# Performance work log

Measured on AMD Instinct MI355X. Metric: run time of the kernel, lower is better.

## Reference

```python
import jax, jax.numpy as jnp
import numpy as np

CHANNELS = [(3, 64), (64, 64), (64, 128), (128, 128), (128, 256), (256, 256), (256, 256),
            (256, 512), (512, 512), (512, 512), (512, 512), (512, 512), (512, 512)]
HW = 256
IN_FEAT = 512 * (HW // 32) * (HW // 32)  # 32768


def _conv(x, w):
    # 3x3, stride 1, pad 1, NCHW / OIHW, no bias
    return jax.lax.conv_general_dilated(x, w, (1, 1), ((1, 1), (1, 1)),
                                         dimension_numbers=("NCHW", "OIHW", "NCHW"))


def _maxpool2(x):
    return jax.lax.reduce_window(x, -jnp.inf, jax.lax.max, (1, 1, 2, 2), (1, 1, 2, 2), "VALID")


def setup_inputs() -> dict:
    key = jax.random.key(0)
    keys = jax.random.split(key, 17)
    inp = {"x": jax.random.normal(keys[0], (1, 3, HW, HW), jnp.float32),
           "H": HW, "W": HW, "nTh": 32, "nTw": 32}
    for i, (cin, cout) in enumerate(CHANNELS):
        scale = (1.0 / np.sqrt(9.0 * cin)).astype(np.float32) if hasattr(np.sqrt(9.0 * cin), 'astype') else 1.0 / np.sqrt(9.0 * cin)
        inp[f"cw{i + 1}"] = jax.random.normal(keys[1 + i], (cout, cin, 3, 3), jnp.float32) * np.float32(1.0 / np.sqrt(9.0 * cin))
    inp["fw1"] = jax.random.normal(keys[14], (4096, IN_FEAT), jnp.float32) * np.float32(1.0 / np.sqrt(IN_FEAT))
    inp["fw2"] = jax.random.normal(keys[15], (4096, 4096), jnp.float32) * np.float32(1.0 / np.sqrt(4096))
    inp["fw3"] = jax.random.normal(keys[16], (1000, 4096), jnp.float32) * np.float32(1.0 / np.sqrt(4096))
    return inp


def reference(x, H, W, nTh, nTw, cw1, cw2, cw3, cw4, cw5, cw6, cw7, cw8, cw9, cw10,
              cw11, cw12, cw13, fw1, fw2, fw3):
    # VGG-16 conv stack; tiling in the original is an execution schedule only,
    # the math equals the untiled stack. conv -> relu repeated, maxpool per block.
    conv_ws = [cw1, cw2, cw3, cw4, cw5, cw6, cw7, cw8, cw9, cw10, cw11, cw12, cw13]
    blocks = [(0, 2), (2, 4), (4, 7), (7, 10), (10, 13)]
    h = x
    for lo, hi in blocks:
        for w in conv_ws[lo:hi]:
            h = jax.nn.relu(_conv(h, w))
        h = _maxpool2(h)
    h = h.reshape(h.shape[0], -1)          # [1, 32768]
    h = h @ fw1.T                           # fc1 (no bias, no relu, as in source)
    h = h @ fw2.T                           # fc2
    h = h @ fw3.T                           # fc3 -> [1, 1000]
    return h
```

## Files before the change

kernel.cpp:

```cpp
#include <hip/hip_runtime.h>
#include <cstddef>


typedef __attribute__((ext_vector_type(8))) short short8;
typedef __attribute__((ext_vector_type(4))) float f32x4;

__device__ inline unsigned short f2bf(float f) {
    unsigned int u = __builtin_bit_cast(unsigned int, f);
    u += 0x7FFF + ((u >> 16) & 1);
    return (unsigned short)(u >> 16);
}
__device__ inline float bf2f(unsigned short h) {
    unsigned int u = ((unsigned int)h) << 16;
    return __builtin_bit_cast(float, u);
}

__global__ void wt_transform_k(const float* __restrict__ w, unsigned short* __restrict__ wt,
                               int Cin, int Cout)
{
    const int co = blockIdx.x, pos = blockIdx.y;
    for (int ci = threadIdx.x; ci < Cin; ci += 64)
        wt[(size_t)(pos * Cout + co) * Cin + ci] = f2bf(w[(size_t)(co * Cin + ci) * 9 + pos]);
}

template<int PR, int MODE>
__global__ __launch_bounds__(256, 2)
void conv_mfma_k(const unsigned short* __restrict__ act,
                 const unsigned short* __restrict__ wt,
                 void* __restrict__ outp,
                 int Cin, int Cout, int H, int W, int chunkCi)
{
    constexpr int NT = PR / 4;
    constexpr int ICELLS = (PR + 2) * 18;
    __shared__ __align__(16) unsigned short wLds[9 * 64 * 32];
    __shared__ __align__(16) unsigned short iLds[ICELLS * 32];

    const int tid = threadIdx.x;
    const int lane = tid & 63, wv = tid >> 6;
    const int half = lane >> 4, l15 = lane & 15;
    const int tilesX = W >> 4;
    const int pY = blockIdx.x / tilesX, pX = blockIdx.x - pY * tilesX;
    const int y0 = pY * PR, x0 = pX * 16;
    const int cob = blockIdx.y, s = blockIdx.z;
    const int ciBeg = s * chunkCi, ciEnd = ciBeg + chunkCi;

    f32x4 acc[4][NT];
#pragma unroll
    for (int mt = 0; mt < 4; ++mt)
#pragma unroll
        for (int nt = 0; nt < NT; ++nt) acc[mt][nt] = (f32x4){0.f, 0.f, 0.f, 0.f};

    for (int ci0 = ciBeg; ci0 < ciEnd; ci0 += 32) {
        __syncthreads();
#pragma unroll
        for (int it = 0; it < 9; ++it) {
            const int idx = it * 256 + tid;
            const int cell = idx >> 2, q = idx & 3;
            const int pos = cell >> 6, co = cell & 63;
            const uint4 v = *(const uint4*)(wt +
                (size_t)(pos * Cout + (cob << 6) + co) * Cin + ci0 + q * 8);
            *(uint4*)&wLds[cell * 32 + q * 8] = v;
        }
#pragma unroll
        for (int it = 0; it < (ICELLS * 4 + 255) / 256; ++it) {
            const int idx = it * 256 + tid;
            if (idx < ICELLS * 4) {
                const int cell = idx >> 2, q = idx & 3;
                const int r = cell / 18, c = cell - r * 18;
                const int y = y0 - 1 + r, x = x0 - 1 + c;
                uint4 v = {0u, 0u, 0u, 0u};
                if (y >= 0 && y < H && x >= 0 && x < W)
                    v = *(const uint4*)(act + (size_t)(y * W + x) * Cin + ci0 + q * 8);
                *(uint4*)&iLds[cell * 32 + q * 8] = v;
            }
        }
        __syncthreads();
#pragma unroll
        for (int ky = 0; ky < 3; ++ky)
#pragma unroll
        for (int kx = 0; kx < 3; ++kx) {
            const int pos = ky * 3 + kx;
            short8 a[4];
#pragma unroll
            for (int mt = 0; mt < 4; ++mt)
                a[mt] = *(const short8*)&wLds[((pos << 6) + (mt << 4) + l15) * 32 + half * 8];
#pragma unroll
            for (int nt = 0; nt < NT; ++nt) {
                const short8 b = *(const short8*)
                    &iLds[((wv * NT + nt + ky) * 18 + l15 + kx) * 32 + half * 8];
#pragma unroll
                for (int mt = 0; mt < 4; ++mt)
                    acc[mt][nt] = __builtin_amdgcn_mfma_f32_16x16x32_bf16(a[mt], b, acc[mt][nt], 0, 0, 0);
            }
        }
    }

    const int xg = x0 + l15;
#pragma unroll
    for (int mt = 0; mt < 4; ++mt)
#pragma unroll
    for (int nt = 0; nt < NT; ++nt) {
        const int yg = y0 + wv * NT + nt;
        const int co = (cob << 6) + (mt << 4) + half * 4;
        const size_t base = (size_t)(yg * W + xg) * Cout + co;
        if (MODE == 2) {
            float4 v = make_float4(acc[mt][nt][0], acc[mt][nt][1], acc[mt][nt][2], acc[mt][nt][3]);
            *(float4*)((float*)outp + (size_t)s * Cout * H * W + base) = v;
        } else {
            ushort4 u;
            u.x = f2bf(MODE == 0 ? fmaxf(acc[mt][nt][0], 0.f) : acc[mt][nt][0]);
            u.y = f2bf(MODE == 0 ? fmaxf(acc[mt][nt][1], 0.f) : acc[mt][nt][1]);
            u.z = f2bf(MODE == 0 ? fmaxf(acc[mt][nt][2], 0.f) : acc[mt][nt][2]);
            u.w = f2bf(MODE == 0 ? fmaxf(acc[mt][nt][3], 0.f) : acc[mt][nt][3]);
            *(ushort4*)((unsigned short*)outp + base) = u;
        }
    }
}

#define TILE 16
#define COB  32
__global__ __launch_bounds__(256)
void conv1_k(const float* __restrict__ in, const float* __restrict__ wt,
             unsigned short* __restrict__ out)
{
    const int Cin = 3, H = 256, W = 256, HW = H * W;
    __shared__ float sIn[2][648];
    __shared__ float sWt[2][768];

    const int tid = threadIdx.x;
    const int bx = blockIdx.x, by = blockIdx.y, co_blk = blockIdx.z;
    const int co_grp = tid >> 6;
    const int lane = tid & 63;
    const int tx = lane & 7, ty = lane >> 3;
    const int x0 = bx * TILE, y0 = by * TILE;

    int iLdsI[3], iG[3], iSub[3]; bool iOk[3];
    int wLdsI[3], wG[3], wSub[3]; bool wOk[3];
#pragma unroll
    for (int j = 0; j < 3; ++j) {
        int i = tid + j * 256;
        iOk[j] = false; iLdsI[j] = 0; iG[j] = 0; iSub[j] = 0;
        if (i < 648) {
            int sub = i / 324; int r = i - sub * 324;
            int iy = r / 18;   int ix = r - iy * 18;
            iSub[j] = sub; iLdsI[j] = sub * 324 + r;
            int y = y0 - 1 + iy, x = x0 - 1 + ix;
            if (y >= 0 && y < H && x >= 0 && x < W) { iOk[j] = true; iG[j] = sub * HW + y * W + x; }
        }
        wOk[j] = false; wLdsI[j] = 0; wG[j] = 0; wSub[j] = 0;
        if (i < 576) {
            int sub = i / 288; int r = i - sub * 288;
            int col = r / 9;   int k = r - col * 9;
            wSub[j] = sub; wLdsI[j] = sub * 384 + col * 12 + k;
            wG[j] = ((co_blk * COB + col) * Cin + sub) * 9 + k;
            wOk[j] = true;
        }
    }

    float4 acc[8];
#pragma unroll
    for (int c = 0; c < 8; ++c) acc[c] = make_float4(0.f, 0.f, 0.f, 0.f);

    const int nSteps = 2;
    float rIn[3], rWt[3];
    {
#pragma unroll
        for (int j = 0; j < 3; ++j)
            rIn[j] = (iOk[j] && iSub[j] < 3) ? in[iG[j]] : 0.f;
#pragma unroll
        for (int j = 0; j < 3; ++j)
            rWt[j] = (wOk[j] && wSub[j] < 3) ? wt[wG[j]] : 0.f;
#pragma unroll
        for (int j = 0; j < 3; ++j) { if (tid + j * 256 < 648) sIn[0][iLdsI[j]] = rIn[j]; }
#pragma unroll
        for (int j = 0; j < 3; ++j) { if (tid + j * 256 < 576) sWt[0][wLdsI[j]] = rWt[j]; }
    }

    for (int t = 0; t < nSteps; ++t) {
        __syncthreads();
        const bool more = (t + 1) < nSteps;
        if (more) {
            const int ci0 = 2;
#pragma unroll
            for (int j = 0; j < 3; ++j)
                rIn[j] = (iOk[j] && (ci0 + iSub[j]) < 3) ? in[(size_t)ci0 * HW + iG[j]] : 0.f;
#pragma unroll
            for (int j = 0; j < 3; ++j)
                rWt[j] = (wOk[j] && (ci0 + wSub[j]) < 3) ? wt[(size_t)ci0 * 9 + wG[j]] : 0.f;
        }
        const int buf = t & 1;
        const float* sI = sIn[buf];
        const float* sW = sWt[buf];
#pragma unroll
        for (int sub = 0; sub < 2; ++sub) {
            float wv[4][4];
            const float* sp = sI + sub * 324 + (2 * ty) * 18 + 2 * tx;
#pragma unroll
            for (int r = 0; r < 4; ++r) {
                float2 a = *(const float2*)(sp + r * 18);
                float2 b = *(const float2*)(sp + r * 18 + 2);
                wv[r][0] = a.x; wv[r][1] = a.y; wv[r][2] = b.x; wv[r][3] = b.y;
            }
#pragma unroll
            for (int c = 0; c < 8; ++c) {
                const float* wp = sW + sub * 384 + (co_grp * 8 + c) * 12;
                float4 w0 = *(const float4*)wp;
                float4 w1 = *(const float4*)(wp + 4);
                float  w8 = wp[8];
                const float wk[9] = {w0.x, w0.y, w0.z, w0.w, w1.x, w1.y, w1.z, w1.w, w8};
                float* ac = (float*)&acc[c];
#pragma unroll
                for (int py = 0; py < 2; ++py)
#pragma unroll
                for (int px = 0; px < 2; ++px) {
                    float sacc = ac[py * 2 + px];
#pragma unroll
                    for (int kk = 0; kk < 9; ++kk)
                        sacc = fmaf(wv[py + kk / 3][px + kk % 3], wk[kk], sacc);
                    ac[py * 2 + px] = sacc;
                }
            }
        }
        if (more) {
#pragma unroll
            for (int j = 0; j < 3; ++j) { if (tid + j * 256 < 648) sIn[buf ^ 1][iLdsI[j]] = rIn[j]; }
#pragma unroll
            for (int j = 0; j < 3; ++j) { if (tid + j * 256 < 576) sWt[buf ^ 1][wLdsI[j]] = rWt[j]; }
        }
    }

    const int co0 = co_blk * COB + co_grp * 8;
#pragma unroll
    for (int py = 0; py < 2; ++py)
#pragma unroll
    for (int px = 0; px < 2; ++px) {
        const int y = y0 + 2 * ty + py, x = x0 + 2 * tx + px;
        unsigned short u8[8];
#pragma unroll
        for (int c = 0; c < 8; ++c)
            u8[c] = f2bf(fmaxf(((const float*)&acc[c])[py * 2 + px], 0.f));
        *(uint4*)(out + (size_t)(y * W + x) * 64 + co0) = *(uint4*)u8;
    }
}

__global__ __launch_bounds__(256)
void pool_cvt_k(const unsigned short* __restrict__ P, unsigned short* __restrict__ out,
                int C, int H, int W)
{
    const int C8 = C >> 3, Wo = W >> 1, Ho = H >> 1;
    const int n = Ho * Wo * C8;
    int i = blockIdx.x * 256 + threadIdx.x;
    if (i >= n) return;
    const int c8 = i % C8, p = i / C8;
    const int yo = p / Wo, xo = p - yo * Wo;
    const size_t b = (size_t)(2 * yo * W + 2 * xo) * C + c8 * 8;
    uint4 a0 = *(const uint4*)(P + b);
    uint4 a1 = *(const uint4*)(P + b + C);
    uint4 a2 = *(const uint4*)(P + b + (size_t)W * C);
    uint4 a3 = *(const uint4*)(P + b + (size_t)W * C + C);
    const unsigned short* s0 = (const unsigned short*)&a0;
    const unsigned short* s1 = (const unsigned short*)&a1;
    const unsigned short* s2 = (const unsigned short*)&a2;
    const unsigned short* s3 = (const unsigned short*)&a3;
    unsigned short u8[8];
#pragma unroll
    for (int k = 0; k < 8; ++k) {
        float m = fmaxf(fmaxf(bf2f(s0[k]), bf2f(s1[k])), fmaxf(bf2f(s2[k]), bf2f(s3[k])));
        u8[k] = f2bf(fmaxf(m, 0.f));
    }
    *(uint4*)(out + (size_t)p * C + c8 * 8) = *(uint4*)u8;
}

__global__ __launch_bounds__(256)
void reduce_cvt_k(const float* __restrict__ P, unsigned short* __restrict__ out,
                  int n4, int S)
{
    int i = blockIdx.x * 256 + threadIdx.x;
    if (i >= n4) return;
    const float4* p4 = (const float4*)P;
    float4 a = p4[i];
    for (int s = 1; s < S; ++s) {
        float4 b = p4[(size_t)i + (size_t)s * n4];
        a.x += b.x; a.y += b.y; a.z += b.z; a.w += b.w;
    }
    ushort4 u;
    u.x = f2bf(fmaxf(a.x, 0.f)); u.y = f2bf(fmaxf(a.y, 0.f));
    u.z = f2bf(fmaxf(a.z, 0.f)); u.w = f2bf(fmaxf(a.w, 0.f));
    *(ushort4*)(out + (size_t)i * 4) = u;
}

__global__ __launch_bounds__(256)
void reduce_pool_cvt_k(const float* __restrict__ P, unsigned short* __restrict__ out,
                       int C, int H, int W, int S)
{
    const int C4 = C >> 2, Wo = W >> 1, Ho = H >> 1;
    const int n = Ho * Wo * C4;
    int i = blockIdx.x * 256 + threadIdx.x;
    if (i >= n) return;
    const int c4 = i % C4, p = i / C4;
    const int yo = p / Wo, xo = p - yo * Wo;
    const size_t CHW = (size_t)C * H * W;
    const size_t b = (size_t)(2 * yo * W + 2 * xo) * C + c4 * 4;
    float4 v[4] = {{0,0,0,0},{0,0,0,0},{0,0,0,0},{0,0,0,0}};
    for (int s = 0; s < S; ++s) {
        const float* ps = P + s * CHW;
        float4 t0 = *(const float4*)(ps + b);
        float4 t1 = *(const float4*)(ps + b + C);
        float4 t2 = *(const float4*)(ps + b + (size_t)W * C);
        float4 t3 = *(const float4*)(ps + b + (size_t)W * C + C);
        v[0].x += t0.x; v[0].y += t0.y; v[0].z += t0.z; v[0].w += t0.w;
        v[1].x += t1.x; v[1].y += t1.y; v[1].z += t1.z; v[1].w += t1.w;
        v[2].x += t2.x; v[2].y += t2.y; v[2].z += t2.z; v[2].w += t2.w;
        v[3].x += t3.x; v[3].y += t3.y; v[3].z += t3.z; v[3].w += t3.w;
    }
    ushort4 u;
    u.x = f2bf(fmaxf(fmaxf(fmaxf(v[0].x, v[1].x), fmaxf(v[2].x, v[3].x)), 0.f));
    u.y = f2bf(fmaxf(fmaxf(fmaxf(v[0].y, v[1].y), fmaxf(v[2].y, v[3].y)), 0.f));
    u.z = f2bf(fmaxf(fmaxf(fmaxf(v[0].z, v[1].z), fmaxf(v[2].z, v[3].z)), 0.f));
    u.w = f2bf(fmaxf(fmaxf(fmaxf(v[0].w, v[1].w), fmaxf(v[2].w, v[3].w)), 0.f));
    *(ushort4*)(out + (size_t)p * C + c4 * 4) = u;
}

__global__ __launch_bounds__(256)
void reduce_pool_f32_k(const float* __restrict__ P, float* __restrict__ out,
                       int C, int H, int W, int S)
{
    const int Wo = W >> 1, Ho = H >> 1;
    const int n = Ho * Wo * C;
    int i = blockIdx.x * 256 + threadIdx.x;
    if (i >= n) return;
    const int c = i % C, p = i / C;
    const int yo = p / Wo, xo = p - yo * Wo;
    const size_t CHW = (size_t)C * H * W;
    float v0 = 0.f, v1 = 0.f, v2 = 0.f, v3 = 0.f;
    const size_t b = (size_t)(2 * yo * W + 2 * xo) * C + c;
    for (int s = 0; s < S; ++s) {
        const float* ps = P + s * CHW;
        v0 += ps[b]; v1 += ps[b + C]; v2 += ps[b + (size_t)W * C]; v3 += ps[b + (size_t)W * C + C];
    }
    out[(size_t)c * (Ho * Wo) + p] = fmaxf(fmaxf(fmaxf(v0, v1), fmaxf(v2, v3)), 0.f);
}

__global__ __launch_bounds__(256)
void gemv_k(const float* __restrict__ Wm, const float* __restrict__ xv,
            float* __restrict__ y, int K)
{
    __shared__ float red[4];
    const int tid = threadIdx.x;
    const float4* row = (const float4*)(Wm + (size_t)blockIdx.x * K);
    const float4* x4  = (const float4*)xv;
    const int K4 = K >> 2;
    float sum = 0.f;
    for (int i = tid; i < K4; i += 256) {
        float4 a = row[i], b = x4[i];
        sum += a.x * b.x + a.y * b.y + a.z * b.z + a.w * b.w;
    }
#pragma unroll
    for (int off = 32; off > 0; off >>= 1) sum += __shfl_down(sum, off, 64);
    if ((tid & 63) == 0) red[tid >> 6] = sum;
    __syncthreads();
    if (tid == 0) y[blockIdx.x] = red[0] + red[1] + red[2] + red[3];
}

extern "C" void kernel_launch(void* const* d_in, const int* in_sizes, int n_in,
                              void* d_out, int out_size, void* d_ws, size_t ws_size,
                              hipStream_t stream)
{
    (void)in_sizes; (void)n_in; (void)out_size; (void)ws_size;
    const float* x = (const float*)d_in[0];
    const float* cw[13];
    for (int i = 0; i < 13; ++i) cw[i] = (const float*)d_in[5 + i];
    const float* fw1 = (const float*)d_in[18];
    const float* fw2 = (const float*)d_in[19];
    const float* fw3 = (const float*)d_in[20];
    float* outp = (float*)d_out;

    static const int CIN[12]  = {64, 64, 128, 128, 256, 256, 256, 512, 512, 512, 512, 512};
    static const int COUT[12] = {64, 128, 128, 256, 256, 256, 512, 512, 512, 512, 512, 512};

    char* ws = (char*)d_ws;
    size_t wOff[12]; size_t o = 0;
    for (int i = 0; i < 12; ++i) { wOff[i] = o; o += (size_t)9 * COUT[i] * CIN[i]; }
    unsigned short* WT = (unsigned short*)ws;
    size_t ao = (o * 2 + 255) & ~(size_t)255;
    unsigned short* bA = (unsigned short*)(ws + ao);
    unsigned short* bB = (unsigned short*)(ws + ao + 8388608);
    char* Pr = ws + ao + 2 * 8388608;
    unsigned short* Pu = (unsigned short*)Pr;
    float* Pf = (float*)Pr;
    float* fcIn = (float*)bA;
    float* F1 = (float*)bB;
    float* F2 = F1 + 4096;

    for (int i = 0; i < 12; ++i)
        wt_transform_k<<<dim3(COUT[i], 9), 64, 0, stream>>>(cw[i + 1], WT + wOff[i], CIN[i], COUT[i]);

    conv1_k<<<dim3(16, 16, 2), 256, 0, stream>>>(x, cw[0], bA);

    conv_mfma_k<16, 1><<<dim3(256, 1, 1), 256, 0, stream>>>(bA, WT + wOff[0], Pu, 64, 64, 256, 256, 64);
    pool_cvt_k<<<(128 * 128 * 8 + 255) / 256, 256, 0, stream>>>(Pu, bB, 64, 256, 256);
    conv_mfma_k<8, 0><<<dim3(128, 2, 1), 256, 0, stream>>>(bB, WT + wOff[1], bA, 64, 128, 128, 128, 64);
    conv_mfma_k<8, 1><<<dim3(128, 2, 1), 256, 0, stream>>>(bA, WT + wOff[2], Pu, 128, 128, 128, 128, 128);
    pool_cvt_k<<<(64 * 64 * 16 + 255) / 256, 256, 0, stream>>>(Pu, bB, 128, 128, 128);
    conv_mfma_k<8, 2><<<dim3(32, 4, 2), 256, 0, stream>>>(bB, WT + wOff[3], Pf, 128, 256, 64, 64, 64);
    reduce_cvt_k<<<(262144 + 255) / 256, 256, 0, stream>>>(Pf, bA, 262144, 2);
    conv_mfma_k<8, 2><<<dim3(32, 4, 2), 256, 0, stream>>>(bA, WT + wOff[4], Pf, 256, 256, 64, 64, 128);
    reduce_cvt_k<<<(262144 + 255) / 256, 256, 0, stream>>>(Pf, bB, 262144, 2);
    conv_mfma_k<8, 2><<<dim3(32, 4, 2), 256, 0, stream>>>(bB, WT + wOff[5], Pf, 256, 256, 64, 64, 128);
    reduce_pool_cvt_k<<<(65536 + 255) / 256, 256, 0, stream>>>(Pf, bA, 256, 64, 64, 2);
    conv_mfma_k<8, 2><<<dim3(8, 8, 4), 256, 0, stream>>>(bA, WT + wOff[6], Pf, 256, 512, 32, 32, 64);
    reduce_cvt_k<<<(131072 + 255) / 256, 256, 0, stream>>>(Pf, bB, 131072, 4);
    conv_mfma_k<8, 2><<<dim3(8, 8, 4), 256, 0, stream>>>(bB, WT + wOff[7], Pf, 512, 512, 32, 32, 128);
    reduce_cvt_k<<<(131072 + 255) / 256, 256, 0, stream>>>(Pf, bA, 131072, 4);
    conv_mfma_k<8, 2><<<dim3(8, 8, 4), 256, 0, stream>>>(bA, WT + wOff[8], Pf, 512, 512, 32, 32, 128);
    reduce_pool_cvt_k<<<(32768 + 255) / 256, 256, 0, stream>>>(Pf, bB, 512, 32, 32, 4);
    conv_mfma_k<8, 2><<<dim3(2, 8, 16), 256, 0, stream>>>(bB, WT + wOff[9], Pf, 512, 512, 16, 16, 32);
    reduce_cvt_k<<<(32768 + 255) / 256, 256, 0, stream>>>(Pf, bA, 32768, 16);
    conv_mfma_k<8, 2><<<dim3(2, 8, 16), 256, 0, stream>>>(bA, WT + wOff[10], Pf, 512, 512, 16, 16, 32);
    reduce_cvt_k<<<(32768 + 255) / 256, 256, 0, stream>>>(Pf, bB, 32768, 16);
    conv_mfma_k<8, 2><<<dim3(2, 8, 16), 256, 0, stream>>>(bB, WT + wOff[11], Pf, 512, 512, 16, 16, 32);
    reduce_pool_f32_k<<<(32768 + 255) / 256, 256, 0, stream>>>(Pf, fcIn, 512, 16, 16, 16);

    gemv_k<<<4096, 256, 0, stream>>>(fw1, fcIn, F1, 32768);
    gemv_k<<<4096, 256, 0, stream>>>(fw2, F1, F2, 4096);
    gemv_k<<<1000, 256, 0, stream>>>(fw3, F2, outp, 4096);
}
```

Baseline: 1.037 ms.

## Double-buffer conv LDS via direct global-to-LDS loads, fuse pooling, batch weight transform

```diff
diff --git a/kernel.cpp b/kernel.cpp
--- a/kernel.cpp
+++ b/kernel.cpp
@@ -15,25 +15,69 @@
     return __builtin_bit_cast(float, u);
 }
 
-__global__ void wt_transform_k(const float* __restrict__ w, unsigned short* __restrict__ wt,
-                               int Cin, int Cout)
-{
-    const int co = blockIdx.x, pos = blockIdx.y;
-    for (int ci = threadIdx.x; ci < Cin; ci += 64)
-        wt[(size_t)(pos * Cout + co) * Cin + ci] = f2bf(w[(size_t)(co * Cin + ci) * 9 + pos]);
+__device__ __forceinline__ void gl_lds16(const void* src, unsigned m0v) {
+    asm volatile("s_mov_b32 m0, %1\n\t"
+                 "global_load_lds_dwordx4 %0, off"
+                 :: "v"(src), "s"(m0v) : "memory");
+}
+
+struct WtDesc { const float* src; unsigned dst; int cin; int cout; int blk0; };
+struct WtArgs { WtDesc d[12]; };
+
+__global__ __launch_bounds__(256)
+void wt_all_k(WtArgs A, unsigned short* __restrict__ wt, unsigned short* __restrict__ guard)
+{
+    __shared__ unsigned short lds[4][9 * 520];
+    const int tid = threadIdx.x, wv = tid >> 6, lane = tid & 63;
+    if (blockIdx.x == 0 && tid < 128) guard[tid] = 0;
+
+    int l = 0;
+#pragma unroll
+    for (int i = 1; i < 12; ++i) l = ((int)blockIdx.x >= A.d[i].blk0) ? i : l;
+    const WtDesc D = A.d[l];
+    const int co = ((int)blockIdx.x - D.blk0) * 4 + wv;
+    const int n = D.cin * 9;
+    const int cinP = D.cin + 8;
+
+    const float4* src = (const float4*)(D.src + (size_t)co * n);
+    for (int i = lane; i < (n >> 2); i += 64) {
+        float4 v = src[i];
+        unsigned short b[4] = {f2bf(v.x), f2bf(v.y), f2bf(v.z), f2bf(v.w)};
+        const int f0 = i * 4;
+#pragma unroll
+        for (int k = 0; k < 4; ++k) {
+            const int f = f0 + k, ci = f / 9, pos = f - ci * 9;
+            lds[wv][pos * cinP + ci] = b[k];
+        }
+    }
+    __syncthreads();
+    unsigned short* dstb = wt + D.dst;
+#pragma unroll 1
+    for (int pos = 0; pos < 9; ++pos) {
+        unsigned short* drow = dstb + ((size_t)pos * D.cout + co) * D.cin;
+        for (int c4 = lane; c4 < (D.cin >> 2); c4 += 64) {
+            ushort4 u = *(const ushort4*)&lds[wv][pos * cinP + c4 * 4];
+            *(ushort4*)(drow + c4 * 4) = u;
+        }
+    }
 }
 
 template<int PR, int MODE>
-__global__ __launch_bounds__(256, 2)
+__global__ __launch_bounds__(256)
 void conv_mfma_k(const unsigned short* __restrict__ act,
                  const unsigned short* __restrict__ wt,
+                 const unsigned short* __restrict__ guard,
                  void* __restrict__ outp,
                  int Cin, int Cout, int H, int W, int chunkCi)
 {
     constexpr int NT = PR / 4;
     constexpr int ICELLS = (PR + 2) * 18;
-    __shared__ __align__(16) unsigned short wLds[9 * 64 * 32];
-    __shared__ __align__(16) unsigned short iLds[ICELLS * 32];
+    constexpr int ITIN = (ICELLS * 4 + 255) / 256;
+    constexpr int VL = 9 + ITIN;
+    static_assert(VL == 12 || VL == 15, "unexpected stage depth");
+
+    __shared__ __align__(16) unsigned short wLds[2][9 * 64 * 32];
+    __shared__ __align__(16) unsigned short iLds[2][ITIN * 2048];
 
     const int tid = threadIdx.x;
     const int lane = tid & 63, wv = tid >> 6;
@@ -42,7 +86,8 @@
     const int pY = blockIdx.x / tilesX, pX = blockIdx.x - pY * tilesX;
     const int y0 = pY * PR, x0 = pX * 16;
     const int cob = blockIdx.y, s = blockIdx.z;
-    const int ciBeg = s * chunkCi, ciEnd = ciBeg + chunkCi;
+    const int ciBeg = s * chunkCi;
+    const int nCh = chunkCi >> 5;
 
     f32x4 acc[4][NT];
 #pragma unroll
@@ -50,31 +95,46 @@
 #pragma unroll
         for (int nt = 0; nt < NT; ++nt) acc[mt][nt] = (f32x4){0.f, 0.f, 0.f, 0.f};
 
-    for (int ci0 = ciBeg; ci0 < ciEnd; ci0 += 32) {
-        __syncthreads();
+    auto STAGE = [&](int buf, int ci0) {
+        const unsigned wB = (unsigned)(size_t)&wLds[buf][0];
+        const unsigned iB = (unsigned)(size_t)&iLds[buf][0];
 #pragma unroll
         for (int it = 0; it < 9; ++it) {
             const int idx = it * 256 + tid;
             const int cell = idx >> 2, q = idx & 3;
             const int pos = cell >> 6, co = cell & 63;
-            const uint4 v = *(const uint4*)(wt +
-                (size_t)(pos * Cout + (cob << 6) + co) * Cin + ci0 + q * 8);
-            *(uint4*)&wLds[cell * 32 + q * 8] = v;
-        }
-#pragma unroll
-        for (int it = 0; it < (ICELLS * 4 + 255) / 256; ++it) {
+            const unsigned short* src = wt +
+                (size_t)(pos * Cout + (cob << 6) + co) * Cin + ci0 + q * 8;
+            gl_lds16(src, __builtin_amdgcn_readfirstlane(wB + (unsigned)(it * 4096 + wv * 1024)));
+        }
+#pragma unroll
+        for (int it = 0; it < ITIN; ++it) {
             const int idx = it * 256 + tid;
-            if (idx < ICELLS * 4) {
-                const int cell = idx >> 2, q = idx & 3;
-                const int r = cell / 18, c = cell - r * 18;
-                const int y = y0 - 1 + r, x = x0 - 1 + c;
-                uint4 v = {0u, 0u, 0u, 0u};
-                if (y >= 0 && y < H && x >= 0 && x < W)
-                    v = *(const uint4*)(act + (size_t)(y * W + x) * Cin + ci0 + q * 8);
-                *(uint4*)&iLds[cell * 32 + q * 8] = v;
-            }
-        }
-        __syncthreads();
+            const int cell = idx >> 2, q = idx & 3;
+            const int r = cell / 18, c = cell - r * 18;
+            const int y = y0 - 1 + r, x = x0 - 1 + c;
+            const bool ok = (idx < ICELLS * 4) & (y >= 0) & (y < H) & (x >= 0) & (x < W);
+            const unsigned short* src = ok ?
+                act + (size_t)(y * W + x) * Cin + ci0 + q * 8 : guard;
+            gl_lds16(src, __builtin_amdgcn_readfirstlane(iB + (unsigned)(it * 4096 + wv * 1024)));
+        }
+    };
+
+    STAGE(0, ciBeg);
+    for (int t = 0; t < nCh; ++t) {
+        const int buf = t & 1;
+        if (t + 1 < nCh) {
+            STAGE(buf ^ 1, ciBeg + ((t + 1) << 5));
+            if constexpr (VL == 12) asm volatile("s_waitcnt vmcnt(12)" ::: "memory");
+            else                    asm volatile("s_waitcnt vmcnt(15)" ::: "memory");
+        } else {
+            asm volatile("s_waitcnt vmcnt(0)" ::: "memory");
+        }
+        __builtin_amdgcn_s_barrier();
+        asm volatile("" ::: "memory");
+
+        const unsigned short* wP = wLds[buf];
+        const unsigned short* iP = iLds[buf];
 #pragma unroll
         for (int ky = 0; ky < 3; ++ky)
 #pragma unroll
@@ -83,36 +143,64 @@
             short8 a[4];
 #pragma unroll
             for (int mt = 0; mt < 4; ++mt)
-                a[mt] = *(const short8*)&wLds[((pos << 6) + (mt << 4) + l15) * 32 + half * 8];
+                a[mt] = *(const short8*)&wP[((pos << 6) + (mt << 4) + l15) * 32 + half * 8];
 #pragma unroll
             for (int nt = 0; nt < NT; ++nt) {
                 const short8 b = *(const short8*)
-                    &iLds[((wv * NT + nt + ky) * 18 + l15 + kx) * 32 + half * 8];
+                    &iP[((wv * NT + nt + ky) * 18 + l15 + kx) * 32 + half * 8];
 #pragma unroll
                 for (int mt = 0; mt < 4; ++mt)
                     acc[mt][nt] = __builtin_amdgcn_mfma_f32_16x16x32_bf16(a[mt], b, acc[mt][nt], 0, 0, 0);
             }
         }
+        asm volatile("" ::: "memory");
+        __builtin_amdgcn_s_barrier();
     }
 
     const int xg = x0 + l15;
-#pragma unroll
-    for (int mt = 0; mt < 4; ++mt)
-#pragma unroll
-    for (int nt = 0; nt < NT; ++nt) {
-        const int yg = y0 + wv * NT + nt;
-        const int co = (cob << 6) + (mt << 4) + half * 4;
-        const size_t base = (size_t)(yg * W + xg) * Cout + co;
-        if (MODE == 2) {
-            float4 v = make_float4(acc[mt][nt][0], acc[mt][nt][1], acc[mt][nt][2], acc[mt][nt][3]);
-            *(float4*)((float*)outp + (size_t)s * Cout * H * W + base) = v;
-        } else {
-            ushort4 u;
-            u.x = f2bf(MODE == 0 ? fmaxf(acc[mt][nt][0], 0.f) : acc[mt][nt][0]);
-            u.y = f2bf(MODE == 0 ? fmaxf(acc[mt][nt][1], 0.f) : acc[mt][nt][1]);
-            u.z = f2bf(MODE == 0 ? fmaxf(acc[mt][nt][2], 0.f) : acc[mt][nt][2]);
-            u.w = f2bf(MODE == 0 ? fmaxf(acc[mt][nt][3], 0.f) : acc[mt][nt][3]);
-            *(ushort4*)((unsigned short*)outp + base) = u;
+    if (MODE == 3) {
+        const int Wo = W >> 1;
+#pragma unroll
+        for (int mt = 0; mt < 4; ++mt)
+#pragma unroll
+        for (int nt = 0; nt < NT; nt += 2) {
+            f32x4 a;
+#pragma unroll
+            for (int j = 0; j < 4; ++j) a[j] = fmaxf(acc[mt][nt][j], acc[mt][nt + 1][j]);
+            f32x4 m;
+#pragma unroll
+            for (int j = 0; j < 4; ++j) m[j] = fmaxf(a[j], __shfl_xor(a[j], 1, 64));
+            if ((l15 & 1) == 0) {
+                const int yo = (y0 + wv * NT + nt) >> 1;
+                const int xo = xg >> 1;
+                const int co = (cob << 6) + (mt << 4) + half * 4;
+                ushort4 u;
+                u.x = f2bf(fmaxf(m[0], 0.f));
+                u.y = f2bf(fmaxf(m[1], 0.f));
+                u.z = f2bf(fmaxf(m[2], 0.f));
+                u.w = f2bf(fmaxf(m[3], 0.f));
+                *(ushort4*)((unsigned short*)outp + ((size_t)(yo * Wo + xo) * Cout + co)) = u;
+            }
+        }
+    } else {
+#pragma unroll
+        for (int mt = 0; mt < 4; ++mt)
+#pragma unroll
+        for (int nt = 0; nt < NT; ++nt) {
+            const int yg = y0 + wv * NT + nt;
+            const int co = (cob << 6) + (mt << 4) + half * 4;
+            const size_t base = (size_t)(yg * W + xg) * Cout + co;
+            if (MODE == 2) {
+                float4 v = make_float4(acc[mt][nt][0], acc[mt][nt][1], acc[mt][nt][2], acc[mt][nt][3]);
+                *(float4*)((float*)outp + (size_t)s * Cout * H * W + base) = v;
+            } else {
+                ushort4 u;
+                u.x = f2bf(fmaxf(acc[mt][nt][0], 0.f));
+                u.y = f2bf(fmaxf(acc[mt][nt][1], 0.f));
+                u.z = f2bf(fmaxf(acc[mt][nt][2], 0.f));
+                u.w = f2bf(fmaxf(acc[mt][nt][3], 0.f));
+                *(ushort4*)((unsigned short*)outp + base) = u;
+            }
         }
     }
 }
@@ -241,34 +329,6 @@
             u8[c] = f2bf(fmaxf(((const float*)&acc[c])[py * 2 + px], 0.f));
         *(uint4*)(out + (size_t)(y * W + x) * 64 + co0) = *(uint4*)u8;
     }
-}
-
-__global__ __launch_bounds__(256)
-void pool_cvt_k(const unsigned short* __restrict__ P, unsigned short* __restrict__ out,
-                int C, int H, int W)
-{
-    const int C8 = C >> 3, Wo = W >> 1, Ho = H >> 1;
-    const int n = Ho * Wo * C8;
-    int i = blockIdx.x * 256 + threadIdx.x;
-    if (i >= n) return;
-    const int c8 = i % C8, p = i / C8;
-    const int yo = p / Wo, xo = p - yo * Wo;
-    const size_t b = (size_t)(2 * yo * W + 2 * xo) * C + c8 * 8;
-    uint4 a0 = *(const uint4*)(P + b);
-    uint4 a1 = *(const uint4*)(P + b + C);
-    uint4 a2 = *(const uint4*)(P + b + (size_t)W * C);
-    uint4 a3 = *(const uint4*)(P + b + (size_t)W * C + C);
-    const unsigned short* s0 = (const unsigned short*)&a0;
-    const unsigned short* s1 = (const unsigned short*)&a1;
-    const unsigned short* s2 = (const unsigned short*)&a2;
-    const unsigned short* s3 = (const unsigned short*)&a3;
-    unsigned short u8[8];
-#pragma unroll
-    for (int k = 0; k < 8; ++k) {
-        float m = fmaxf(fmaxf(bf2f(s0[k]), bf2f(s1[k])), fmaxf(bf2f(s2[k]), bf2f(s3[k])));
-        u8[k] = f2bf(fmaxf(m, 0.f));
-    }
-    *(uint4*)(out + (size_t)p * C + c8 * 8) = *(uint4*)u8;
 }
 
 __global__ __launch_bounds__(256)
@@ -382,43 +442,53 @@
     size_t wOff[12]; size_t o = 0;
     for (int i = 0; i < 12; ++i) { wOff[i] = o; o += (size_t)9 * COUT[i] * CIN[i]; }
     unsigned short* WT = (unsigned short*)ws;
-    size_t ao = (o * 2 + 255) & ~(size_t)255;
+    unsigned short* guardp = WT + o;
+    size_t ao = ((o + 128) * 2 + 255) & ~(size_t)255;
     unsigned short* bA = (unsigned short*)(ws + ao);
     unsigned short* bB = (unsigned short*)(ws + ao + 8388608);
     char* Pr = ws + ao + 2 * 8388608;
-    unsigned short* Pu = (unsigned short*)Pr;
     float* Pf = (float*)Pr;
     float* fcIn = (float*)bA;
     float* F1 = (float*)bB;
     float* F2 = F1 + 4096;
 
-    for (int i = 0; i < 12; ++i)
-        wt_transform_k<<<dim3(COUT[i], 9), 64, 0, stream>>>(cw[i + 1], WT + wOff[i], CIN[i], COUT[i]);
+    WtArgs wa; int blk = 0;
+    {
+        size_t oo = 0;
+        for (int i = 0; i < 12; ++i) {
+            wa.d[i].src = cw[i + 1];
+            wa.d[i].dst = (unsigned)oo;
+            wa.d[i].cin = CIN[i];
+            wa.d[i].cout = COUT[i];
+            wa.d[i].blk0 = blk;
+            oo += (size_t)9 * COUT[i] * CIN[i];
+            blk += COUT[i] / 4;
+        }
+    }
+    wt_all_k<<<blk, 256, 0, stream>>>(wa, WT, guardp);
 
     conv1_k<<<dim3(16, 16, 2), 256, 0, stream>>>(x, cw[0], bA);
 
-    conv_mfma_k<16, 1><<<dim3(256, 1, 1), 256, 0, stream>>>(bA, WT + wOff[0], Pu, 64, 64, 256, 256, 64);
-    pool_cvt_k<<<(128 * 128 * 8 + 255) / 256, 256, 0, stream>>>(Pu, bB, 64, 256, 256);
-    conv_mfma_k<8, 0><<<dim3(128, 2, 1), 256, 0, stream>>>(bB, WT + wOff[1], bA, 64, 128, 128, 128, 64);
-    conv_mfma_k<8, 1><<<dim3(128, 2, 1), 256, 0, stream>>>(bA, WT + wOff[2], Pu, 128, 128, 128, 128, 128);
-    pool_cvt_k<<<(64 * 64 * 16 + 255) / 256, 256, 0, stream>>>(Pu, bB, 128, 128, 128);
-    conv_mfma_k<8, 2><<<dim3(32, 4, 2), 256, 0, stream>>>(bB, WT + wOff[3], Pf, 128, 256, 64, 64, 64);
+    conv_mfma_k<16, 3><<<dim3(256, 1, 1), 256, 0, stream>>>(bA, WT + wOff[0], guardp, bB, 64, 64, 256, 256, 64);
+    conv_mfma_k<8, 0><<<dim3(128, 2, 1), 256, 0, stream>>>(bB, WT + wOff[1], guardp, bA, 64, 128, 128, 128, 64);
+    conv_mfma_k<8, 3><<<dim3(128, 2, 1), 256, 0, stream>>>(bA, WT + wOff[2], guardp, bB, 128, 128, 128, 128, 128);
+    conv_mfma_k<8, 2><<<dim3(32, 4, 2), 256, 0, stream>>>(bB, WT + wOff[3], guardp, Pf, 128, 256, 64, 64, 64);
     reduce_cvt_k<<<(262144 + 255) / 256, 256, 0, stream>>>(Pf, bA, 262144, 2);
-    conv_mfma_k<8, 2><<<dim3(32, 4, 2), 256, 0, stream>>>(bA, WT + wOff[4], Pf, 256, 256, 64, 64, 128);
+    conv_mfma_k<8, 2><<<dim3(32, 4, 2), 256, 0, stream>>>(bA, WT + wOff[4], guardp, Pf, 256, 256, 64, 64, 128);
     reduce_cvt_k<<<(262144 + 255) / 256, 256, 0, stream>>>(Pf, bB, 262144, 2);
-    conv_mfma_k<8, 2><<<dim3(32, 4, 2), 256, 0, stream>>>(bB, WT + wOff[5], Pf, 256, 256, 64, 64, 128);
+    conv_mfma_k<8, 2><<<dim3(32, 4, 2), 256, 0, stream>>>(bB, WT + wOff[5], guardp, Pf, 256, 256, 64, 64, 128);
     reduce_pool_cvt_k<<<(65536 + 255) / 256, 256, 0, stream>>>(Pf, bA, 256, 64, 64, 2);
-    conv_mfma_k<8, 2><<<dim3(8, 8, 4), 256, 0, stream>>>(bA, WT + wOff[6], Pf, 256, 512, 32, 32, 64);
+    conv_mfma_k<8, 2><<<dim3(8, 8, 4), 256, 0, stream>>>(bA, WT + wOff[6], guardp, Pf, 256, 512, 32, 32, 64);
     reduce_cvt_k<<<(131072 + 255) / 256, 256, 0, stream>>>(Pf, bB, 131072, 4);
-    conv_mfma_k<8, 2><<<dim3(8, 8, 4), 256, 0, stream>>>(bB, WT + wOff[7], Pf, 512, 512, 32, 32, 128);
+    conv_mfma_k<8, 2><<<dim3(8, 8, 4), 256, 0, stream>>>(bB, WT + wOff[7], guardp, Pf, 512, 512, 32, 32, 128);
     reduce_cvt_k<<<(131072 + 255) / 256, 256, 0, stream>>>(Pf, bA, 131072, 4);
-    conv_mfma_k<8, 2><<<dim3(8, 8, 4), 256, 0, stream>>>(bA, WT + wOff[8], Pf, 512, 512, 32, 32, 128);
+    conv_mfma_k<8, 2><<<dim3(8, 8, 4), 256, 0, stream>>>(bA, WT + wOff[8], guardp, Pf, 512, 512, 32, 32, 128);
     reduce_pool_cvt_k<<<(32768 + 255) / 256, 256, 0, stream>>>(Pf, bB, 512, 32, 32, 4);
-    conv_mfma_k<8, 2><<<dim3(2, 8, 16), 256, 0, stream>>>(bB, WT + wOff[9], Pf, 512, 512, 16, 16, 32);
+    conv_mfma_k<8, 2><<<dim3(2, 8, 16), 256, 0, stream>>>(bB, WT + wOff[9], guardp, Pf, 512, 512, 16, 16, 32);
     reduce_cvt_k<<<(32768 + 255) / 256, 256, 0, stream>>>(Pf, bA, 32768, 16);
-    conv_mfma_k<8, 2><<<dim3(2, 8, 16), 256, 0, stream>>>(bA, WT + wOff[10], Pf, 512, 512, 16, 16, 32);
+    conv_mfma_k<8, 2><<<dim3(2, 8, 16), 256, 0, stream>>>(bA, WT + wOff[10], guardp, Pf, 512, 512, 16, 16, 32);
     reduce_cvt_k<<<(32768 + 255) / 256, 256, 0, stream>>>(Pf, bB, 32768, 16);
-    conv_mfma_k<8, 2><<<dim3(2, 8, 16), 256, 0, stream>>>(bB, WT + wOff[11], Pf, 512, 512, 16, 16, 32);
+    conv_mfma_k<8, 2><<<dim3(2, 8, 16), 256, 0, stream>>>(bB, WT + wOff[11], guardp, Pf, 512, 512, 16, 16, 32);
     reduce_pool_f32_k<<<(32768 + 255) / 256, 256, 0, stream>>>(Pf, fcIn, 512, 16, 16, 16);
 
     gemv_k<<<4096, 256, 0, stream>>>(fw1, fcIn, F1, 32768);
```

Result: faster. 972.6 us (-6.2%).
